# Optimization experiments

Measured on AMD Instinct MI355X. Metric: run time of the kernel, lower is better.

The kernel has to match this reference:

```python
import jax, jax.numpy as jnp
import numpy as np

B, N_MELS, T = 8, 96, 1024
FLUX = 1
N_DIMS = N_MELS * (1 + FLUX)          # 192
C = 32                                 # num_channels
D_MODEL = C * (N_DIMS // 4)            # 1536
N_LAYERS = 4
D_STATE = 16
D_CONV = 4
D_INNER = 2 * D_MODEL                  # 3072 (expand=2)
DT_RANK = -(-D_MODEL // 16)            # 96
N_CLASSES = 5


def setup_inputs() -> dict:
    key = jax.random.key(0)
    ks = iter(jax.random.split(key, 64))
    def rn(shape, scale=0.02):
        return jax.random.normal(next(ks), shape, dtype=jnp.float32) * scale
    p = {}
    p['x'] = jax.random.normal(next(ks), (B, N_MELS, T), dtype=jnp.float32)
    # ResidualBlock 1: conv3x3 -> act -> conv3x3, 1x1 shortcut (channel change 1->C)
    p['c1a_w'] = rn((C, 1, 3, 3)); p['c1a_b'] = jnp.zeros((C,), jnp.float32)
    p['c1b_w'] = rn((C, C, 3, 3)); p['c1b_b'] = jnp.zeros((C,), jnp.float32)
    p['c1s_w'] = rn((C, 1, 1, 1)); p['c1s_b'] = jnp.zeros((C,), jnp.float32)
    # ResidualBlock 2: identity shortcut (C->C)
    p['c2a_w'] = rn((C, C, 3, 3)); p['c2a_b'] = jnp.zeros((C,), jnp.float32)
    p['c2b_w'] = rn((C, C, 3, 3)); p['c2b_b'] = jnp.zeros((C,), jnp.float32)
    # Mamba layers (stacked over layer dim L)
    L = N_LAYERS
    p['norm_w'] = jnp.ones((L, D_MODEL), jnp.float32)
    p['in_w'] = rn((L, 2 * D_INNER, D_MODEL))
    p['conv_w'] = rn((L, D_INNER, D_CONV))
    p['conv_b'] = jnp.zeros((L, D_INNER), jnp.float32)
    p['xproj_w'] = rn((L, DT_RANK + 2 * D_STATE, D_INNER))
    p['dt_w'] = rn((L, D_INNER, DT_RANK))
    p['dt_b'] = rn((L, D_INNER), 0.01)
    A = jnp.tile(jnp.arange(1, D_STATE + 1, dtype=jnp.float32)[None], (D_INNER, 1))
    p['A_log'] = jnp.tile(jnp.log(A)[None], (L, 1, 1))
    p['Dp'] = jnp.ones((L, D_INNER), jnp.float32)
    p['out_w'] = rn((L, D_MODEL, D_INNER))
    p['fc_w'] = rn((N_CLASSES, D_MODEL)); p['fc_b'] = jnp.zeros((N_CLASSES,), jnp.float32)
    return p


def conv2d_same(x, w, b):
    y = jax.lax.conv_general_dilated(x, w, (1, 1), 'SAME',
                                     dimension_numbers=('NCHW', 'OIHW', 'NCHW'))
    return y + b[None, :, None, None]


def res_block(x, wa, ba, wb, bb, ws=None, bs=None):
    h = jax.nn.silu(conv2d_same(x, wa, ba))
    h = conv2d_same(h, wb, bb)
    sc = x if ws is None else conv2d_same(x, ws, bs)
    return jax.nn.silu(h + sc)


def maxpool_f2(x):
    # MaxPool2d(kernel=(2,1), stride=(2,1)) over (freq, time)
    return jax.lax.reduce_window(x, -jnp.inf, jax.lax.max,
                                 (1, 1, 2, 1), (1, 1, 2, 1), 'VALID')


def rmsnorm(x, w, eps=1e-5):
    return x * jax.lax.rsqrt(jnp.mean(x * x, -1, keepdims=True) + eps) * w


def mamba_layer(x, norm_w, in_w, conv_w, conv_b, xproj_w, dt_w, dt_b, A_log, Dp, out_w):
    # x: (B, T, D_MODEL)
    xn = rmsnorm(x, norm_w)
    xz = jnp.einsum('btd,ed->bte', xn, in_w)           # (B,T,2*d_inner)
    u, z = jnp.split(xz, 2, axis=-1)
    # depthwise causal conv over time
    u_t = jnp.transpose(u, (0, 2, 1))                   # (B, d_inner, T)
    u_t = jax.lax.conv_general_dilated(u_t, conv_w[:, None, :], (1,), [(D_CONV - 1, 0)],
                                       dimension_numbers=('NCH', 'OIH', 'NCH'),
                                       feature_group_count=D_INNER)
    u = jax.nn.silu(jnp.transpose(u_t, (0, 2, 1)) + conv_b)
    x_dbl = jnp.einsum('btd,ed->bte', u, xproj_w)
    dt, Bm, Cm = jnp.split(x_dbl, [DT_RANK, DT_RANK + D_STATE], axis=-1)
    delta = jax.nn.softplus(jnp.einsum('btr,dr->btd', dt, dt_w) + dt_b)  # (B,T,d_inner)
    A = -jnp.exp(A_log)                                 # (d_inner, d_state)

    def step(h, inp):
        d_t, u_tt, B_t, C_t = inp                        # (B,di),(B,di),(B,ds),(B,ds)
        dA = jnp.exp(d_t[..., None] * A)                 # (B, d_inner, d_state)
        h = dA * h + (d_t * u_tt)[..., None] * B_t[:, None, :]
        y = jnp.einsum('bds,bs->bd', h, C_t)
        return h, y

    h0 = jnp.zeros((x.shape[0], D_INNER, D_STATE), x.dtype)
    xs = (jnp.moveaxis(delta, 1, 0), jnp.moveaxis(u, 1, 0),
          jnp.moveaxis(Bm, 1, 0), jnp.moveaxis(Cm, 1, 0))
    _, ys = jax.lax.scan(step, h0, xs)
    y = jnp.moveaxis(ys, 0, 1) + u * Dp
    y = y * jax.nn.silu(z)
    return x + jnp.einsum('bte,de->btd', y, out_w)


def reference(x, c1a_w, c1a_b, c1b_w, c1b_b, c1s_w, c1s_b,
              c2a_w, c2a_b, c2b_w, c2b_b,
              norm_w, in_w, conv_w, conv_b, xproj_w, dt_w, dt_b, A_log, Dp, out_w,
              fc_w, fc_b):
    # flux: temporal diff, relu, left-pad on time, stack along freq
    diff = x[..., 1:] - x[..., :-1]
    diff = jax.nn.relu(jnp.pad(diff, ((0, 0), (0, 0), (1, 0))))
    h = jnp.concatenate([x, diff], axis=1)              # (B, n_dims, T)
    h = h[:, None]                                       # (B, 1, n_dims, T)
    h = maxpool_f2(res_block(h, c1a_w, c1a_b, c1b_w, c1b_b, c1s_w, c1s_b))
    h = maxpool_f2(res_block(h, c2a_w, c2a_b, c2b_w, c2b_b))
    h = h.reshape(h.shape[0], -1, h.shape[3])            # (B, C*(n_dims//4), T)
    h = jnp.transpose(h, (0, 2, 1))                      # (B, T, d_model)
    for l in range(N_LAYERS):
        h = mamba_layer(h, norm_w[l], in_w[l], conv_w[l], conv_b[l], xproj_w[l],
                        dt_w[l], dt_b[l], A_log[l], Dp[l], out_w[l])
    logits = jnp.einsum('btd,cd->btc', h, fc_w) + fc_b
    return jax.nn.silu(jnp.transpose(logits, (0, 2, 1)))  # (B, n_classes, T)
```

## Files before the change

kernel.cpp:

```cpp
#include <hip/hip_runtime.h>
#include <cstdint>
#include <cstddef>

#define DEV static __device__ __forceinline__

typedef unsigned short u16;
typedef unsigned int   u32;
typedef __bf16 bf16x8 __attribute__((ext_vector_type(8)));
typedef float  f32x4  __attribute__((ext_vector_type(4)));

namespace {
constexpr int NB     = 8;
constexpr int NT     = 1024;
constexpr int NMEL   = 96;
constexpr int NDIM   = 192;
constexpr int NCH    = 32;
constexpr int DMODEL = 1536;
constexpr int DINNER = 3072;
constexpr int DSTATE = 16;
constexpr int DTRANK = 96;
constexpr int NLAYER = 4;
constexpr int NCLASS = 5;
constexpr int MROWS  = NB * NT;
constexpr int NCHK   = 16;
constexpr int CHKT   = NT / NCHK;
}

DEV float siluf(float x)    { return x / (1.0f + __expf(-x)); }
DEV float softplusf(float x){ return fmaxf(x, 0.0f) + log1pf(__expf(-fabsf(x))); }

DEV u16 f2bf(float f) {
    u32 u = __float_as_uint(f);
    u32 r = u + 0x7FFFu + ((u >> 16) & 1u);
    return (u16)(r >> 16);
}
DEV float bf2f(u16 h) { return __uint_as_float(((u32)h) << 16); }

DEV f32x4 exp2v(f32x4 x) {
    f32x4 r;
    r[0] = exp2f(x[0]); r[1] = exp2f(x[1]);
    r[2] = exp2f(x[2]); r[3] = exp2f(x[3]);
    return r;
}

#define GLD(gp, lp) __builtin_amdgcn_global_load_lds( \
    (const __attribute__((address_space(1))) u32*)(const void*)(gp), \
    (__attribute__((address_space(3))) u32*)(void*)(lp), 16, 0, 0)

__global__ void k_zero(u16* p) { p[threadIdx.x] = 0; }

__global__ __launch_bounds__(256) void k_prep(const float* __restrict__ x,
                                              float* __restrict__ hcat)
{
    int idx = blockIdx.x * 256 + threadIdx.x;
    if (idx >= NB * NDIM * NT) return;
    int t = idx & (NT - 1);
    int m = (idx >> 10) % NDIM;
    int b = idx / (NDIM * NT);
    float v;
    if (m < NMEL) {
        v = x[((size_t)b * NMEL + m) * NT + t];
    } else {
        int mm = m - NMEL;
        v = 0.f;
        if (t > 0) {
            const float* p = x + ((size_t)b * NMEL + mm) * NT + t;
            v = fmaxf(p[0] - p[-1], 0.f);
        }
    }
    hcat[idx] = v;
}

__global__ __launch_bounds__(256) void k_wconv(const float* __restrict__ w,
    u16* __restrict__ dh, u16* __restrict__ dl)
{
    int idx = blockIdx.x * 256 + threadIdx.x;
    if (idx >= 9216) return;
    int ci = idx & 31, cout = (idx >> 5) & 31, tap = idx >> 10;
    float v = w[((size_t)cout * 32 + ci) * 9 + tap];
    u16 h = f2bf(v);
    dh[idx] = h;
    dl[idx] = f2bf(v - bf2f(h));
}

__global__ __launch_bounds__(256) void k_conv1a(const float* __restrict__ hcat,
    const float* __restrict__ w, const float* __restrict__ bias,
    u16* __restrict__ oh, u16* __restrict__ ol)
{
    int idx = blockIdx.x * 256 + threadIdx.x;
    if (idx >= NB * NDIM * NT) return;
    int t = idx & (NT - 1);
    int h = (idx >> 10) % NDIM;
    int b = idx / (NDIM * NT);
    float in[3][3];
    #pragma unroll
    for (int dh = 0; dh < 3; ++dh)
        #pragma unroll
        for (int dw = 0; dw < 3; ++dw) {
            int hh = h + dh - 1, tt = t + dw - 1;
            in[dh][dw] = (hh >= 0 && hh < NDIM && tt >= 0 && tt < NT)
                       ? hcat[((size_t)b * NDIM + hh) * NT + tt] : 0.f;
        }
    u16 hb[32], lb[32];
    #pragma unroll
    for (int c = 0; c < NCH; ++c) {
        float acc = bias[c];
        #pragma unroll
        for (int dh = 0; dh < 3; ++dh)
            #pragma unroll
            for (int dw = 0; dw < 3; ++dw)
                acc = fmaf(in[dh][dw], w[c * 9 + dh * 3 + dw], acc);
        float o = siluf(acc);
        u16 hh2 = f2bf(o);
        hb[c] = hh2;
        lb[c] = f2bf(o - bf2f(hh2));
    }
    size_t ob = (((size_t)b * NDIM + h) * NT + t) * 32;
    #pragma unroll
    for (int j = 0; j < 8; ++j) {
        ushort4 hv = { hb[j*4], hb[j*4+1], hb[j*4+2], hb[j*4+3] };
        ushort4 lv = { lb[j*4], lb[j*4+1], lb[j*4+2], lb[j*4+3] };
        *(ushort4*)(oh + ob + j * 4) = hv;
        *(ushort4*)(ol + ob + j * 4) = lv;
    }
}

template<int VAR>
__global__ __launch_bounds__(256) void k_convmfma(
    const u16* __restrict__ Xh, const u16* __restrict__ Xl,
    const u16* __restrict__ CWh, const u16* __restrict__ CWl,
    const float* __restrict__ hcat, const float* __restrict__ sw, const float* __restrict__ sb,
    const u16* __restrict__ Sh, const u16* __restrict__ Sl,
    const float* __restrict__ bias,
    u16* __restrict__ Oh, u16* __restrict__ Ol,
    float* __restrict__ RES,
    const u16* __restrict__ zeropad)
{
    constexpr int HIN = (VAR == 0) ? 192 : 96;
    __shared__ __align__(16) u16 lds[2][8448];
    const int t0 = blockIdx.x * 64;
    const int ho = blockIdx.y;
    const int b  = blockIdx.z;
    const int tid = threadIdx.x;
    const int wid = tid >> 6, lane = tid & 63;
    const int r0 = 2 * ho - 1;

    for (int cb = wid * 64; cb < 2112; cb += 256) {
        int c = cb + lane;
        int plane = (c >= 1056) ? 1 : 0;
        int cc = c - plane * 1056;
        int row = cc / 264;
        int rc  = cc - row * 264;
        int pos = rc >> 2;
        int slot = rc & 3;
        int cib = slot ^ ((pos >> 1) & 3);
        int h = r0 + row;
        int t = t0 - 1 + pos;
        const u16* bp = plane ? Xl : Xh;
        const u16* src = (h >= 0 && h < HIN && t >= 0 && t < NT)
            ? bp + (((size_t)(b * HIN + h)) * NT + t) * 32 + cib * 8
            : zeropad;
        u16* ldst = &lds[0][0] + (size_t)cb * 8;
        GLD(src, ldst);
    }
    __syncthreads();

    const int fr = lane & 15, fq = lane >> 4;
    f32x4 acc[2][2];
    #pragma unroll
    for (int pr = 0; pr < 2; ++pr)
        #pragma unroll
        for (int mt = 0; mt < 2; ++mt) acc[pr][mt] = (f32x4){0.f, 0.f, 0.f, 0.f};

    #pragma unroll
    for (int dh = 0; dh < 3; ++dh) {
        #pragma unroll
        for (int dt = 0; dt < 3; ++dt) {
            int tap = dh * 3 + dt;
            bf16x8 wh[2], wl[2];
            #pragma unroll
            for (int mt = 0; mt < 2; ++mt) {
                size_t wo = ((size_t)tap * 32 + mt * 16 + fr) * 32 + fq * 8;
                wh[mt] = *(const bf16x8*)(CWh + wo);
                wl[mt] = *(const bf16x8*)(CWl + wo);
            }
            int p = (wid << 4) + fr + dt;
            int sl = fq ^ ((p >> 1) & 3);
            #pragma unroll
            for (int pr = 0; pr < 2; ++pr) {
                int rr = pr + dh;
                const u16* lp = &lds[0][0] + ((rr * 66 + p) * 4 + sl) * 8;
                bf16x8 xh = *(const bf16x8*)lp;
                bf16x8 xl = *(const bf16x8*)(lp + 8448);
                #pragma unroll
                for (int mt = 0; mt < 2; ++mt) {
                    acc[pr][mt] = __builtin_amdgcn_mfma_f32_16x16x32_bf16(wh[mt], xh, acc[pr][mt], 0, 0, 0);
                    acc[pr][mt] = __builtin_amdgcn_mfma_f32_16x16x32_bf16(wh[mt], xl, acc[pr][mt], 0, 0, 0);
                    acc[pr][mt] = __builtin_amdgcn_mfma_f32_16x16x32_bf16(wl[mt], xh, acc[pr][mt], 0, 0, 0);
                }
            }
        }
    }

    const int t = t0 + (wid << 4) + fr;
    float hc0 = 0.f, hc1 = 0.f;
    if (VAR == 0) {
        hc0 = hcat[((size_t)(b * NDIM + 2 * ho    )) * NT + t];
        hc1 = hcat[((size_t)(b * NDIM + 2 * ho + 1)) * NT + t];
    }
    #pragma unroll
    for (int mt = 0; mt < 2; ++mt) {
        float v0[4], v1[4];
        if (VAR == 2) {
            ushort4 s0h = *(const ushort4*)(Sh + (((size_t)(b * 96 + 2 * ho    )) * NT + t) * 32 + mt * 16 + fq * 4);
            ushort4 s0l = *(const ushort4*)(Sl + (((size_t)(b * 96 + 2 * ho    )) * NT + t) * 32 + mt * 16 + fq * 4);
            ushort4 s1h = *(const ushort4*)(Sh + (((size_t)(b * 96 + 2 * ho + 1)) * NT + t) * 32 + mt * 16 + fq * 4);
            ushort4 s1l = *(const ushort4*)(Sl + (((size_t)(b * 96 + 2 * ho + 1)) * NT + t) * 32 + mt * 16 + fq * 4);
            v0[0] = bf2f(s0h.x) + bf2f(s0l.x); v0[1] = bf2f(s0h.y) + bf2f(s0l.y);
            v0[2] = bf2f(s0h.z) + bf2f(s0l.z); v0[3] = bf2f(s0h.w) + bf2f(s0l.w);
            v1[0] = bf2f(s1h.x) + bf2f(s1l.x); v1[1] = bf2f(s1h.y) + bf2f(s1l.y);
            v1[2] = bf2f(s1h.z) + bf2f(s1l.z); v1[3] = bf2f(s1h.w) + bf2f(s1l.w);
        }
        u16 hs[4], ls[4];
        float r0v[4], r1v[4];
        #pragma unroll
        for (int r = 0; r < 4; ++r) {
            int c = mt * 16 + fq * 4 + r;
            float a0 = acc[0][mt][r] + bias[c];
            float a1 = acc[1][mt][r] + bias[c];
            if (VAR == 0) {
                a0 += fmaf(hc0, sw[c], sb[c]);
                a1 += fmaf(hc1, sw[c], sb[c]);
            }
            if (VAR == 2) { a0 += v0[r]; a1 += v1[r]; }
            a0 = siluf(a0); a1 = siluf(a1);
            if (VAR == 1) { r0v[r] = a0; r1v[r] = a1; }
            else {
                float m = fmaxf(a0, a1);
                if (VAR == 2) r0v[r] = m;
                else { u16 hh = f2bf(m); hs[r] = hh; ls[r] = f2bf(m - bf2f(hh)); }
            }
        }
        if (VAR == 0) {
            size_t ob = (((size_t)(b * 96 + ho)) * NT + t) * 32 + mt * 16 + fq * 4;
            ushort4 hv = { hs[0], hs[1], hs[2], hs[3] };
            ushort4 lv = { ls[0], ls[1], ls[2], ls[3] };
            *(ushort4*)(Oh + ob) = hv;
            *(ushort4*)(Ol + ob) = lv;
        } else if (VAR == 1) {
            #pragma unroll
            for (int pr = 0; pr < 2; ++pr) {
                size_t ob = (((size_t)(b * 96 + 2 * ho + pr)) * NT + t) * 32 + mt * 16 + fq * 4;
                u16 hh[4], ll[4];
                #pragma unroll
                for (int r = 0; r < 4; ++r) {
                    float m = pr ? r1v[r] : r0v[r];
                    hh[r] = f2bf(m); ll[r] = f2bf(m - bf2f(hh[r]));
                }
                ushort4 hv = { hh[0], hh[1], hh[2], hh[3] };
                ushort4 lv = { ll[0], ll[1], ll[2], ll[3] };
                *(ushort4*)(Oh + ob) = hv;
                *(ushort4*)(Ol + ob) = lv;
            }
        } else {
            #pragma unroll
            for (int r = 0; r < 4; ++r) {
                int c = mt * 16 + fq * 4 + r;
                RES[((size_t)b * NT + t) * DMODEL + c * 48 + ho] = r0v[r];
            }
        }
    }
}

__global__ __launch_bounds__(256) void k_rmsnorm(const float* __restrict__ in,
    const float* __restrict__ w, u16* __restrict__ oh, u16* __restrict__ ol)
{
    int row = blockIdx.x;
    int tid = threadIdx.x;
    const float* p = in + (size_t)row * DMODEL;
    float v[6]; float ss = 0.f;
    #pragma unroll
    for (int j = 0; j < 6; ++j) { v[j] = p[tid + j * 256]; ss = fmaf(v[j], v[j], ss); }
    #pragma unroll
    for (int off = 1; off < 64; off <<= 1) ss += __shfl_xor(ss, off);
    __shared__ float red[4];
    int lane = tid & 63, wv = tid >> 6;
    if (lane == 0) red[wv] = ss;
    __syncthreads();
    float tot = red[0] + red[1] + red[2] + red[3];
    float sc = rsqrtf(tot * (1.0f / DMODEL) + 1e-5f);
    #pragma unroll
    for (int j = 0; j < 6; ++j) {
        int col = tid + j * 256;
        float xv = v[j] * sc * w[col];
        u16 h = f2bf(xv);
        oh[(size_t)row * DMODEL + col] = h;
        ol[(size_t)row * DMODEL + col] = f2bf(xv - bf2f(h));
    }
}

__global__ __launch_bounds__(256) void k_split(const float* __restrict__ src,
    u16* __restrict__ dh, u16* __restrict__ dl, int n4)
{
    int idx = blockIdx.x * 256 + threadIdx.x;
    if (idx >= n4) return;
    float4 v = ((const float4*)src)[idx];
    u16 h0 = f2bf(v.x), h1 = f2bf(v.y), h2 = f2bf(v.z), h3 = f2bf(v.w);
    u16 l0 = f2bf(v.x - bf2f(h0)), l1 = f2bf(v.y - bf2f(h1));
    u16 l2 = f2bf(v.z - bf2f(h2)), l3 = f2bf(v.w - bf2f(h3));
    uint2 hv = { (u32)h0 | ((u32)h1 << 16), (u32)h2 | ((u32)h3 << 16) };
    uint2 lv = { (u32)l0 | ((u32)l1 << 16), (u32)l2 | ((u32)l3 << 16) };
    ((uint2*)dh)[idx] = hv;
    ((uint2*)dl)[idx] = lv;
}

__global__ __launch_bounds__(256) void k_wsplit_pad(const float* __restrict__ src,
    u16* __restrict__ dh, u16* __restrict__ dl)
{
    int idx = blockIdx.x * 256 + threadIdx.x;
    if (idx >= DINNER * 128) return;
    int col = idx & 127, row = idx >> 7;
    float v = (col < DTRANK) ? src[(size_t)row * DTRANK + col] : 0.f;
    u16 h = f2bf(v);
    dh[idx] = h;
    dl[idx] = f2bf(v - bf2f(h));
}

template<int EPI>
__global__ __launch_bounds__(256) void k_gemm_mfma(
    const u16* __restrict__ Ahi, const u16* __restrict__ Alo, int lda,
    const u16* __restrict__ Bhi, const u16* __restrict__ Blo, int ldb,
    float* __restrict__ C, int ldc, int Ktot,
    const float* __restrict__ bias, size_t zStride)
{
    __shared__ __align__(16) u16 lds[4][8192];
    const int tid = threadIdx.x;
    const int m0 = blockIdx.y * 128, n0 = blockIdx.x * 128;
    const int kPer = Ktot / gridDim.z;
    const int kBase = blockIdx.z * kPer;
    const int wid = tid >> 6, lane = tid & 63;
    const int wr = wid >> 1, wc = wid & 1;
    const int fr = lane & 15, fq = lane >> 4;
    const int srow  = tid >> 3;
    const int sslot = (tid & 7) ^ ((tid >> 3) & 7);

    f32x4 acc[4][4];
    #pragma unroll
    for (int mi = 0; mi < 4; ++mi)
        #pragma unroll
        for (int ni = 0; ni < 4; ++ni) acc[mi][ni] = (f32x4){0.f, 0.f, 0.f, 0.f};

    for (int k0 = kBase; k0 < kBase + kPer; k0 += 64) {
        #pragma unroll
        for (int i = 0; i < 4; ++i) {
            int row = i * 32 + srow;
            size_t offA = (size_t)(m0 + row) * lda + k0 + sslot * 8;
            size_t offB = (size_t)(n0 + row) * ldb + k0 + sslot * 8;
            u16* lb = &lds[0][0] + i * 2048 + (wid << 9);
            GLD(Ahi + offA, lb);
            GLD(Alo + offA, lb + 8192);
            GLD(Bhi + offB, lb + 16384);
            GLD(Blo + offB, lb + 24576);
        }
        __syncthreads();
        #pragma unroll
        for (int h = 0; h < 2; ++h) {
            bf16x8 ah[4], al[4], bh[4], bl[4];
            #pragma unroll
            for (int mi = 0; mi < 4; ++mi) {
                int row = wr * 64 + mi * 16 + fr;
                int sl  = (h * 4 + fq) ^ (row & 7);
                const u16* p = &lds[0][row * 64 + sl * 8];
                ah[mi] = *(const bf16x8*)p;
                al[mi] = *(const bf16x8*)(p + 8192);
            }
            #pragma unroll
            for (int ni = 0; ni < 4; ++ni) {
                int row = wc * 64 + ni * 16 + fr;
                int sl  = (h * 4 + fq) ^ (row & 7);
                const u16* p = &lds[2][row * 64 + sl * 8];
                bh[ni] = *(const bf16x8*)p;
                bl[ni] = *(const bf16x8*)(p + 8192);
            }
            #pragma unroll
            for (int mi = 0; mi < 4; ++mi)
                #pragma unroll
                for (int ni = 0; ni < 4; ++ni) {
                    acc[mi][ni] = __builtin_amdgcn_mfma_f32_16x16x32_bf16(ah[mi], bh[ni], acc[mi][ni], 0, 0, 0);
                    acc[mi][ni] = __builtin_amdgcn_mfma_f32_16x16x32_bf16(ah[mi], bl[ni], acc[mi][ni], 0, 0, 0);
                    acc[mi][ni] = __builtin_amdgcn_mfma_f32_16x16x32_bf16(al[mi], bh[ni], acc[mi][ni], 0, 0, 0);
                }
        }
        __syncthreads();
    }

    float* Cz = C + (EPI == 0 ? (size_t)blockIdx.z * zStride : (size_t)0);
    #pragma unroll
    for (int mi = 0; mi < 4; ++mi)
        #pragma unroll
        for (int ni = 0; ni < 4; ++ni) {
            int gr = m0 + wr * 64 + mi * 16 + fq * 4;
            int gc = n0 + wc * 64 + ni * 16 + fr;
            float* cp = Cz + (size_t)gr * ldc + gc;
            #pragma unroll
            for (int r = 0; r < 4; ++r) {
                float v = acc[mi][ni][r];
                if (EPI == 1) v = softplusf(v + bias[gc]);
                if (EPI == 2) v += cp[(size_t)r * ldc];
                cp[(size_t)r * ldc] = v;
            }
        }
}

__global__ __launch_bounds__(256) void k_conv1d(
    const float* __restrict__ xz, const float* __restrict__ w,
    const float* __restrict__ bias, u16* __restrict__ uh, u16* __restrict__ ul)
{
    int idx = blockIdx.x * 256 + threadIdx.x;
    if (idx >= NB * NT * (DINNER / 4)) return;
    int dv = idx % (DINNER / 4);
    int t  = (idx / (DINNER / 4)) % NT;
    int b  = idx / ((DINNER / 4) * NT);
    int d  = dv * 4;
    const float* base = xz + ((size_t)b * NT + t) * (2 * DINNER) + d;
    float4 a[4];
    #pragma unroll
    for (int k = 0; k < 4; ++k) {
        int tm = t - 3 + k;
        if (tm >= 0) a[k] = *(const float4*)(base + (ptrdiff_t)(k - 3) * (2 * DINNER));
        else         a[k] = make_float4(0.f, 0.f, 0.f, 0.f);
    }
    float4 w0 = *(const float4*)(w + (size_t)(d + 0) * 4);
    float4 w1 = *(const float4*)(w + (size_t)(d + 1) * 4);
    float4 w2 = *(const float4*)(w + (size_t)(d + 2) * 4);
    float4 w3 = *(const float4*)(w + (size_t)(d + 3) * 4);
    float4 bb = *(const float4*)(bias + d);
    float o0 = siluf(bb.x + a[0].x * w0.x + a[1].x * w0.y + a[2].x * w0.z + a[3].x * w0.w);
    float o1 = siluf(bb.y + a[0].y * w1.x + a[1].y * w1.y + a[2].y * w1.z + a[3].y * w1.w);
    float o2 = siluf(bb.z + a[0].z * w2.x + a[1].z * w2.y + a[2].z * w2.z + a[3].z * w2.w);
    float o3 = siluf(bb.w + a[0].w * w3.x + a[1].w * w3.y + a[2].w * w3.z + a[3].w * w3.w);
    u16 h0 = f2bf(o0), h1 = f2bf(o1), h2 = f2bf(o2), h3 = f2bf(o3);
    u16 l0 = f2bf(o0 - bf2f(h0)), l1 = f2bf(o1 - bf2f(h1));
    u16 l2 = f2bf(o2 - bf2f(h2)), l3 = f2bf(o3 - bf2f(h3));
    size_t ob = ((size_t)b * NT + t) * DINNER + d;
    uint2 hv = { (u32)h0 | ((u32)h1 << 16), (u32)h2 | ((u32)h3 << 16) };
    uint2 lv = { (u32)l0 | ((u32)l1 << 16), (u32)l2 | ((u32)l3 << 16) };
    *(uint2*)(uh + ob) = hv;
    *(uint2*)(ul + ob) = lv;
}

__global__ __launch_bounds__(256) void k_reduce4(const float* __restrict__ part,
                                                 float* __restrict__ out)
{
    int idx = blockIdx.x * 256 + threadIdx.x;
    if (idx >= MROWS * 128) return;
    float s = part[idx] + part[(size_t)1 * MROWS * 128 + idx]
            + part[(size_t)2 * MROWS * 128 + idx] + part[(size_t)3 * MROWS * 128 + idx];
    out[idx] = s;
}

__global__ __launch_bounds__(256) void k_scan_p1(
    const float* __restrict__ xz, const u16* __restrict__ uh, const u16* __restrict__ ul,
    const float* __restrict__ xdbl, const float* __restrict__ A_log,
    float* __restrict__ HP, float* __restrict__ SS)
{
    const int d = blockIdx.x * 256 + threadIdx.x;
    const int c = blockIdx.y, b = blockIdx.z;
    const float L2E = 1.44269504088896340736f;
    f32x4 al0 = *(const f32x4*)(A_log + (size_t)d * DSTATE + 0);
    f32x4 al1 = *(const f32x4*)(A_log + (size_t)d * DSTATE + 4);
    f32x4 al2 = *(const f32x4*)(A_log + (size_t)d * DSTATE + 8);
    f32x4 al3 = *(const f32x4*)(A_log + (size_t)d * DSTATE + 12);
    f32x4 aa0, aa1, aa2, aa3;
    #pragma unroll
    for (int j = 0; j < 4; ++j) {
        aa0[j] = -__expf(al0[j]) * L2E;
        aa1[j] = -__expf(al1[j]) * L2E;
        aa2[j] = -__expf(al2[j]) * L2E;
        aa3[j] = -__expf(al3[j]) * L2E;
    }
    const int t0 = c * CHKT;
    const float* dP = xz + ((size_t)b * NT + t0) * (2 * DINNER) + d;
    const u16* uhP = uh + ((size_t)b * NT + t0) * DINNER + d;
    const u16* ulP = ul + ((size_t)b * NT + t0) * DINNER + d;
    const float* bP = xdbl + ((size_t)b * NT + t0) * 128 + DTRANK;
    f32x4 h0 = {0.f,0.f,0.f,0.f}, h1 = h0, h2 = h0, h3 = h0;
    float S = 0.f;
    float dlt = dP[0];
    float uu = bf2f(uhP[0]) + bf2f(ulP[0]);
    for (int t = 0; t < CHKT; ++t) {
        float dlt_n = 0.f, uu_n = 0.f;
        if (t + 1 < CHKT) {
            dlt_n = dP[2 * DINNER];
            uu_n = bf2f(uhP[DINNER]) + bf2f(ulP[DINNER]);
        }
        f32x4 B0 = *(const f32x4*)(bP + 0);
        f32x4 B1 = *(const f32x4*)(bP + 4);
        f32x4 B2 = *(const f32x4*)(bP + 8);
        f32x4 B3 = *(const f32x4*)(bP + 12);
        float du = dlt * uu;
        S += dlt;
        h0 = exp2v(dlt * aa0) * h0 + du * B0;
        h1 = exp2v(dlt * aa1) * h1 + du * B1;
        h2 = exp2v(dlt * aa2) * h2 + du * B2;
        h3 = exp2v(dlt * aa3) * h3 + du * B3;
        dP += 2 * DINNER; uhP += DINNER; ulP += DINNER; bP += 128;
        dlt = dlt_n; uu = uu_n;
    }
    size_t a = (((size_t)(b * NCHK + c) * DINNER) + d) * DSTATE;
    *(f32x4*)(HP + a + 0)  = h0;
    *(f32x4*)(HP + a + 4)  = h1;
    *(f32x4*)(HP + a + 8)  = h2;
    *(f32x4*)(HP + a + 12) = h3;
    SS[(size_t)(b * NCHK + c) * DINNER + d] = S;
}

__global__ __launch_bounds__(256) void k_scan_p2(float* __restrict__ HP,
    const float* __restrict__ SS, const float* __restrict__ A_log)
{
    int idx = blockIdx.x * 256 + threadIdx.x;
    if (idx >= NB * DINNER * DSTATE) return;
    int s = idx & (DSTATE - 1);
    int d = (idx >> 4) % DINNER;
    int b = idx / (DINNER * DSTATE);
    const float L2E = 1.44269504088896340736f;
    float aa = -__expf(A_log[d * DSTATE + s]) * L2E;
    float h = 0.f;
    #pragma unroll
    for (int c = 0; c < NCHK; ++c) {
        size_t a = (((size_t)(b * NCHK + c) * DINNER) + d) * DSTATE + s;
        float hc = HP[a];
        float P = exp2f(aa * SS[(size_t)(b * NCHK + c) * DINNER + d]);
        HP[a] = h;
        h = fmaf(P, h, hc);
    }
}

__global__ __launch_bounds__(256) void k_scan_p3(
    const float* __restrict__ xz,
    u16* uh, u16* ul,
    const float* __restrict__ xdbl,
    const float* __restrict__ A_log, const float* __restrict__ Dp,
    const float* __restrict__ HP)
{
    const int d = blockIdx.x * 256 + threadIdx.x;
    const int c = blockIdx.y, b = blockIdx.z;
    const float L2E = 1.44269504088896340736f;
    f32x4 al0 = *(const f32x4*)(A_log + (size_t)d * DSTATE + 0);
    f32x4 al1 = *(const f32x4*)(A_log + (size_t)d * DSTATE + 4);
    f32x4 al2 = *(const f32x4*)(A_log + (size_t)d * DSTATE + 8);
    f32x4 al3 = *(const f32x4*)(A_log + (size_t)d * DSTATE + 12);
    f32x4 aa0, aa1, aa2, aa3;
    #pragma unroll
    for (int j = 0; j < 4; ++j) {
        aa0[j] = -__expf(al0[j]) * L2E;
        aa1[j] = -__expf(al1[j]) * L2E;
        aa2[j] = -__expf(al2[j]) * L2E;
        aa3[j] = -__expf(al3[j]) * L2E;
    }
    const float dp = Dp[d];
    const int t0 = c * CHKT;
    const float* dP = xz + ((size_t)b * NT + t0) * (2 * DINNER) + d;
    const float* zP = dP + DINNER;
    const u16* uhP = uh + ((size_t)b * NT + t0) * DINNER + d;
    const u16* ulP = ul + ((size_t)b * NT + t0) * DINNER + d;
    u16* yhP = (u16*)uhP;
    u16* ylP = (u16*)ulP;
    const float* bP = xdbl + ((size_t)b * NT + t0) * 128 + DTRANK;
    size_t ha = (((size_t)(b * NCHK + c) * DINNER) + d) * DSTATE;
    f32x4 h0 = *(const f32x4*)(HP + ha + 0);
    f32x4 h1 = *(const f32x4*)(HP + ha + 4);
    f32x4 h2 = *(const f32x4*)(HP + ha + 8);
    f32x4 h3 = *(const f32x4*)(HP + ha + 12);
    float dlt = dP[0], zz = zP[0];
    float uu = bf2f(uhP[0]) + bf2f(ulP[0]);
    for (int t = 0; t < CHKT; ++t) {
        float dlt_n = 0.f, uu_n = 0.f, zz_n = 0.f;
        if (t + 1 < CHKT) {
            dlt_n = dP[2 * DINNER]; zz_n = zP[2 * DINNER];
            uu_n = bf2f(uhP[DINNER]) + bf2f(ulP[DINNER]);
        }
        f32x4 B0 = *(const f32x4*)(bP + 0);
        f32x4 B1 = *(const f32x4*)(bP + 4);
        f32x4 B2 = *(const f32x4*)(bP + 8);
        f32x4 B3 = *(const f32x4*)(bP + 12);
        f32x4 C0 = *(const f32x4*)(bP + DSTATE + 0);
        f32x4 C1 = *(const f32x4*)(bP + DSTATE + 4);
        f32x4 C2 = *(const f32x4*)(bP + DSTATE + 8);
        f32x4 C3 = *(const f32x4*)(bP + DSTATE + 12);
        float du = dlt * uu;
        h0 = exp2v(dlt * aa0) * h0 + du * B0;
        h1 = exp2v(dlt * aa1) * h1 + du * B1;
        h2 = exp2v(dlt * aa2) * h2 + du * B2;
        h3 = exp2v(dlt * aa3) * h3 + du * B3;
        f32x4 pv = h0 * C0 + h1 * C1 + h2 * C2 + h3 * C3;
        float p = (pv[0] + pv[1]) + (pv[2] + pv[3]);
        float yv = (p + uu * dp) * siluf(zz);
        u16 hh = f2bf(yv);
        yhP[0] = hh;
        ylP[0] = f2bf(yv - bf2f(hh));
        dP += 2 * DINNER; zP += 2 * DINNER;
        uhP += DINNER; ulP += DINNER; yhP += DINNER; ylP += DINNER;
        bP += 128;
        dlt = dlt_n; zz = zz_n; uu = uu_n;
    }
}

__global__ __launch_bounds__(256) void k_fc(const float* __restrict__ hR,
    const float* __restrict__ w, const float* __restrict__ bias,
    float* __restrict__ out)
{
    int row = blockIdx.x;
    int tid = threadIdx.x;
    const float* p = hR + (size_t)row * DMODEL;
    float acc[NCLASS] = {0.f, 0.f, 0.f, 0.f, 0.f};
    #pragma unroll
    for (int j = 0; j < 6; ++j) {
        int col = tid + j * 256;
        float v = p[col];
        #pragma unroll
        for (int c = 0; c < NCLASS; ++c)
            acc[c] = fmaf(v, w[c * DMODEL + col], acc[c]);
    }
    #pragma unroll
    for (int c = 0; c < NCLASS; ++c)
        #pragma unroll
        for (int off = 1; off < 64; off <<= 1)
            acc[c] += __shfl_xor(acc[c], off);
    __shared__ float red[4][NCLASS];
    int lane = tid & 63, wv = tid >> 6;
    if (lane == 0)
        for (int c = 0; c < NCLASS; ++c) red[wv][c] = acc[c];
    __syncthreads();
    if (tid < NCLASS) {
        float s = red[0][tid] + red[1][tid] + red[2][tid] + red[3][tid] + bias[tid];
        int b = row >> 10, t = row & (NT - 1);
        out[((size_t)b * NCLASS + tid) * NT + t] = siluf(s);
    }
}

extern "C" void kernel_launch(void* const* d_in, const int* in_sizes, int n_in,
                              void* d_out, int out_size, void* d_ws, size_t ws_size,
                              hipStream_t stream)
{
    const float* x      = (const float*)d_in[0];
    const float* c1a_w  = (const float*)d_in[1];
    const float* c1a_b  = (const float*)d_in[2];
    const float* c1b_w  = (const float*)d_in[3];
    const float* c1b_b  = (const float*)d_in[4];
    const float* c1s_w  = (const float*)d_in[5];
    const float* c1s_b  = (const float*)d_in[6];
    const float* c2a_w  = (const float*)d_in[7];
    const float* c2a_b  = (const float*)d_in[8];
    const float* c2b_w  = (const float*)d_in[9];
    const float* c2b_b  = (const float*)d_in[10];
    const float* norm_w = (const float*)d_in[11];
    const float* in_w   = (const float*)d_in[12];
    const float* conv_w = (const float*)d_in[13];
    const float* conv_b = (const float*)d_in[14];
    const float* xproj_w= (const float*)d_in[15];
    const float* dt_w   = (const float*)d_in[16];
    const float* dt_b   = (const float*)d_in[17];
    const float* A_log  = (const float*)d_in[18];
    const float* Dp     = (const float*)d_in[19];
    const float* out_w  = (const float*)d_in[20];
    const float* fc_w   = (const float*)d_in[21];
    const float* fc_b   = (const float*)d_in[22];
    float* outp = (float*)d_out;
    (void)in_sizes; (void)n_in; (void)out_size; (void)ws_size;

    char* base = (char*)d_ws;
    size_t off = 0;
    auto takeB = [&](size_t bytes) { void* p = base + off; off = (off + bytes + 255) & ~(size_t)255; return p; };
    float* HCAT = (float*)takeB((size_t)NB * NDIM * NT * 4);
    float* XZ   = (float*)takeB((size_t)MROWS * 2 * DINNER * 4);
    float* RES  = (float*)takeB((size_t)MROWS * DMODEL * 4);
    u16*   XNh  = (u16*)takeB((size_t)MROWS * DMODEL * 2);
    u16*   XNl  = (u16*)takeB((size_t)MROWS * DMODEL * 2);
    u16*   Uh   = (u16*)takeB((size_t)MROWS * DINNER * 2);
    u16*   Ul   = (u16*)takeB((size_t)MROWS * DINNER * 2);
    float* XDBL = (float*)takeB((size_t)MROWS * 128 * 4);
    float* XPART= (float*)takeB((size_t)4 * MROWS * 128 * 4);
    u16*   XDh  = (u16*)takeB((size_t)MROWS * 128 * 2);
    u16*   XDl  = (u16*)takeB((size_t)MROWS * 128 * 2);
    u16*   Wh   = (u16*)takeB((size_t)9437184 * 2);
    u16*   Wl   = (u16*)takeB((size_t)9437184 * 2);
    float* HP   = (float*)takeB((size_t)NB * NCHK * DINNER * DSTATE * 4);
    float* SS   = (float*)takeB((size_t)NB * NCHK * DINNER * 4);
    u16*   CW1h = (u16*)takeB(18432);
    u16*   CW1l = (u16*)takeB(18432);
    u16*   CW2h = (u16*)takeB(18432);
    u16*   CW2l = (u16*)takeB(18432);
    u16*   CW3h = (u16*)takeB(18432);
    u16*   CW3l = (u16*)takeB(18432);
    u16*   ZPAD = (u16*)takeB(256);

    u16* T1h = (u16*)XZ;
    u16* T1l = T1h + (size_t)NB * NDIM * NT * 32;
    u16* T3h = (u16*)XZ;
    u16* T3l = T3h + (size_t)NB * NDIM * NT * 32;
    u16* P1h = Uh;
    u16* P1l = Ul;

    const int n1 = NB * NDIM * NT;
    k_zero<<<1, 128, 0, stream>>>(ZPAD);
    k_prep  <<<(n1 + 255) / 256, 256, 0, stream>>>(x, HCAT);
    k_wconv<<<36, 256, 0, stream>>>(c1b_w, CW1h, CW1l);
    k_wconv<<<36, 256, 0, stream>>>(c2a_w, CW2h, CW2l);
    k_wconv<<<36, 256, 0, stream>>>(c2b_w, CW3h, CW3l);
    k_conv1a<<<(n1 + 255) / 256, 256, 0, stream>>>(HCAT, c1a_w, c1a_b, T1h, T1l);
    k_convmfma<0><<<dim3(16, 96, NB), 256, 0, stream>>>(
        T1h, T1l, CW1h, CW1l, HCAT, c1s_w, c1s_b, nullptr, nullptr,
        c1b_b, P1h, P1l, nullptr, ZPAD);
    k_convmfma<1><<<dim3(16, 48, NB), 256, 0, stream>>>(
        P1h, P1l, CW2h, CW2l, nullptr, nullptr, nullptr, nullptr, nullptr,
        c2a_b, T3h, T3l, nullptr, ZPAD);
    k_convmfma<2><<<dim3(16, 48, NB), 256, 0, stream>>>(
        T3h, T3l, CW3h, CW3l, nullptr, nullptr, nullptr, P1h, P1l,
        c2b_b, nullptr, nullptr, RES, ZPAD);

    for (int l = 0; l < NLAYER; ++l) {
        k_rmsnorm<<<MROWS, 256, 0, stream>>>(RES, norm_w + (size_t)l * DMODEL, XNh, XNl);
        k_split<<<(9437184 / 4 + 255) / 256, 256, 0, stream>>>(
            in_w + (size_t)l * 2 * DINNER * DMODEL, Wh, Wl, 9437184 / 4);
        k_gemm_mfma<0><<<dim3(2 * DINNER / 128, MROWS / 128, 1), 256, 0, stream>>>(
            XNh, XNl, DMODEL, Wh, Wl, DMODEL, XZ, 2 * DINNER, DMODEL, nullptr, 0);
        k_conv1d<<<(NB * NT * (DINNER / 4) + 255) / 256, 256, 0, stream>>>(
            XZ, conv_w + (size_t)l * DINNER * 4, conv_b + (size_t)l * DINNER, Uh, Ul);
        k_split<<<(393216 / 4 + 255) / 256, 256, 0, stream>>>(
            xproj_w + (size_t)l * 128 * DINNER, Wh, Wl, 393216 / 4);
        k_gemm_mfma<0><<<dim3(1, MROWS / 128, 4), 256, 0, stream>>>(
            Uh, Ul, DINNER, Wh, Wl, DINNER, XPART, 128, DINNER, nullptr, (size_t)MROWS * 128);
        k_reduce4<<<(MROWS * 128 + 255) / 256, 256, 0, stream>>>(XPART, XDBL);
        k_split<<<(MROWS * 128 / 4 + 255) / 256, 256, 0, stream>>>(XDBL, XDh, XDl, MROWS * 128 / 4);
        k_wsplit_pad<<<(DINNER * 128 + 255) / 256, 256, 0, stream>>>(
            dt_w + (size_t)l * DINNER * DTRANK, Wh, Wl);
        k_gemm_mfma<1><<<dim3(DINNER / 128, MROWS / 128, 1), 256, 0, stream>>>(
            XDh, XDl, 128, Wh, Wl, 128, XZ, 2 * DINNER, 128,
            dt_b + (size_t)l * DINNER, 0);
        k_scan_p1<<<dim3(DINNER / 256, NCHK, NB), 256, 0, stream>>>(
            XZ, Uh, Ul, XDBL, A_log + (size_t)l * DINNER * DSTATE, HP, SS);
        k_scan_p2<<<(NB * DINNER * DSTATE + 255) / 256, 256, 0, stream>>>(
            HP, SS, A_log + (size_t)l * DINNER * DSTATE);
        k_scan_p3<<<dim3(DINNER / 256, NCHK, NB), 256, 0, stream>>>(
            XZ, Uh, Ul, XDBL, A_log + (size_t)l * DINNER * DSTATE,
            Dp + (size_t)l * DINNER, HP);
        k_split<<<(4718592 / 4 + 255) / 256, 256, 0, stream>>>(
            out_w + (size_t)l * DMODEL * DINNER, Wh, Wl, 4718592 / 4);
        k_gemm_mfma<2><<<dim3(DMODEL / 128, MROWS / 128, 1), 256, 0, stream>>>(
            Uh, Ul, DINNER, Wh, Wl, DINNER, RES, DMODEL, DINNER, nullptr, 0);
    }
    k_fc<<<MROWS, 256, 0, stream>>>(RES, fc_w, fc_b, outp);
}
```

Before: 5.280 ms.

## Halve GEMM K-tile for occupancy, swizzle block order, retile depthwise conv1d over time

The split-bf16 MFMA GEMM now uses a 32-wide K step with half the LDS, an adjusted XOR swizzle and a launch-bounds hint of 4 blocks per CU, to allow more resident blocks. It also remaps block indices with a modulo-8 swizzle for better L2 locality. The depthwise conv1d now has each thread walk 16 consecutive timesteps for 2 channels, keeping a sliding window in registers instead of reloading 4 rows per output. The trade-off is twice as many barriers per K in the GEMM and possible register pressure under the new launch bound.

```diff
diff --git a/kernel.cpp b/kernel.cpp
--- a/kernel.cpp
+++ b/kernel.cpp
@@ -327,22 +327,27 @@
 }
 
 template<int EPI>
-__global__ __launch_bounds__(256) void k_gemm_mfma(
+__global__ __launch_bounds__(256, 4) void k_gemm_mfma(
     const u16* __restrict__ Ahi, const u16* __restrict__ Alo, int lda,
     const u16* __restrict__ Bhi, const u16* __restrict__ Blo, int ldb,
     float* __restrict__ C, int ldc, int Ktot,
     const float* __restrict__ bias, size_t zStride)
 {
-    __shared__ __align__(16) u16 lds[4][8192];
+    __shared__ __align__(16) u16 lds[4][4096];
     const int tid = threadIdx.x;
-    const int m0 = blockIdx.y * 128, n0 = blockIdx.x * 128;
+    const int nxy = gridDim.x * gridDim.y;
+    const int lin = blockIdx.y * gridDim.x + blockIdx.x;
+    const int swz = (lin & 7) * (nxy >> 3) + (lin >> 3);
+    const int bx = swz % gridDim.x;
+    const int by = swz / gridDim.x;
+    const int m0 = by * 128, n0 = bx * 128;
     const int kPer = Ktot / gridDim.z;
     const int kBase = blockIdx.z * kPer;
     const int wid = tid >> 6, lane = tid & 63;
     const int wr = wid >> 1, wc = wid & 1;
     const int fr = lane & 15, fq = lane >> 4;
-    const int srow  = tid >> 3;
-    const int sslot = (tid & 7) ^ ((tid >> 3) & 7);
+    const int srow  = tid >> 2;
+    const int sslot = (tid & 3) ^ ((srow >> 1) & 3);
 
     f32x4 acc[4][4];
     #pragma unroll
@@ -350,47 +355,44 @@
         #pragma unroll
         for (int ni = 0; ni < 4; ++ni) acc[mi][ni] = (f32x4){0.f, 0.f, 0.f, 0.f};
 
-    for (int k0 = kBase; k0 < kBase + kPer; k0 += 64) {
-        #pragma unroll
-        for (int i = 0; i < 4; ++i) {
-            int row = i * 32 + srow;
+    for (int k0 = kBase; k0 < kBase + kPer; k0 += 32) {
+        #pragma unroll
+        for (int i = 0; i < 2; ++i) {
+            int row = i * 64 + srow;
             size_t offA = (size_t)(m0 + row) * lda + k0 + sslot * 8;
             size_t offB = (size_t)(n0 + row) * ldb + k0 + sslot * 8;
             u16* lb = &lds[0][0] + i * 2048 + (wid << 9);
             GLD(Ahi + offA, lb);
-            GLD(Alo + offA, lb + 8192);
-            GLD(Bhi + offB, lb + 16384);
-            GLD(Blo + offB, lb + 24576);
+            GLD(Alo + offA, lb + 4096);
+            GLD(Bhi + offB, lb + 8192);
+            GLD(Blo + offB, lb + 12288);
         }
         __syncthreads();
-        #pragma unroll
-        for (int h = 0; h < 2; ++h) {
-            bf16x8 ah[4], al[4], bh[4], bl[4];
-            #pragma unroll
-            for (int mi = 0; mi < 4; ++mi) {
-                int row = wr * 64 + mi * 16 + fr;
-                int sl  = (h * 4 + fq) ^ (row & 7);
-                const u16* p = &lds[0][row * 64 + sl * 8];
-                ah[mi] = *(const bf16x8*)p;
-                al[mi] = *(const bf16x8*)(p + 8192);
-            }
+        bf16x8 ah[4], al[4], bh[4], bl[4];
+        #pragma unroll
+        for (int mi = 0; mi < 4; ++mi) {
+            int row = wr * 64 + mi * 16 + fr;
+            int sl  = fq ^ ((row >> 1) & 3);
+            const u16* p = &lds[0][row * 32 + sl * 8];
+            ah[mi] = *(const bf16x8*)p;
+            al[mi] = *(const bf16x8*)(p + 4096);
+        }
+        #pragma unroll
+        for (int ni = 0; ni < 4; ++ni) {
+            int row = wc * 64 + ni * 16 + fr;
+            int sl  = fq ^ ((row >> 1) & 3);
+            const u16* p = &lds[2][row * 32 + sl * 8];
+            bh[ni] = *(const bf16x8*)p;
+            bl[ni] = *(const bf16x8*)(p + 4096);
+        }
+        #pragma unroll
+        for (int mi = 0; mi < 4; ++mi)
             #pragma unroll
             for (int ni = 0; ni < 4; ++ni) {
-                int row = wc * 64 + ni * 16 + fr;
-                int sl  = (h * 4 + fq) ^ (row & 7);
-                const u16* p = &lds[2][row * 64 + sl * 8];
-                bh[ni] = *(const bf16x8*)p;
-                bl[ni] = *(const bf16x8*)(p + 8192);
+                acc[mi][ni] = __builtin_amdgcn_mfma_f32_16x16x32_bf16(ah[mi], bh[ni], acc[mi][ni], 0, 0, 0);
+                acc[mi][ni] = __builtin_amdgcn_mfma_f32_16x16x32_bf16(ah[mi], bl[ni], acc[mi][ni], 0, 0, 0);
+                acc[mi][ni] = __builtin_amdgcn_mfma_f32_16x16x32_bf16(al[mi], bh[ni], acc[mi][ni], 0, 0, 0);
             }
-            #pragma unroll
-            for (int mi = 0; mi < 4; ++mi)
-                #pragma unroll
-                for (int ni = 0; ni < 4; ++ni) {
-                    acc[mi][ni] = __builtin_amdgcn_mfma_f32_16x16x32_bf16(ah[mi], bh[ni], acc[mi][ni], 0, 0, 0);
-                    acc[mi][ni] = __builtin_amdgcn_mfma_f32_16x16x32_bf16(ah[mi], bl[ni], acc[mi][ni], 0, 0, 0);
-                    acc[mi][ni] = __builtin_amdgcn_mfma_f32_16x16x32_bf16(al[mi], bh[ni], acc[mi][ni], 0, 0, 0);
-                }
-        }
         __syncthreads();
     }
 
@@ -416,37 +418,33 @@
     const float* __restrict__ xz, const float* __restrict__ w,
     const float* __restrict__ bias, u16* __restrict__ uh, u16* __restrict__ ul)
 {
-    int idx = blockIdx.x * 256 + threadIdx.x;
-    if (idx >= NB * NT * (DINNER / 4)) return;
-    int dv = idx % (DINNER / 4);
-    int t  = (idx / (DINNER / 4)) % NT;
-    int b  = idx / ((DINNER / 4) * NT);
-    int d  = dv * 4;
-    const float* base = xz + ((size_t)b * NT + t) * (2 * DINNER) + d;
-    float4 a[4];
-    #pragma unroll
-    for (int k = 0; k < 4; ++k) {
-        int tm = t - 3 + k;
-        if (tm >= 0) a[k] = *(const float4*)(base + (ptrdiff_t)(k - 3) * (2 * DINNER));
-        else         a[k] = make_float4(0.f, 0.f, 0.f, 0.f);
-    }
-    float4 w0 = *(const float4*)(w + (size_t)(d + 0) * 4);
+    constexpr int CT = 16;
+    const int d  = (blockIdx.x * 256 + threadIdx.x) * 2;
+    const int t0 = blockIdx.y * CT;
+    const int b  = blockIdx.z;
+    float4 w0 = *(const float4*)(w + (size_t)d * 4);
     float4 w1 = *(const float4*)(w + (size_t)(d + 1) * 4);
-    float4 w2 = *(const float4*)(w + (size_t)(d + 2) * 4);
-    float4 w3 = *(const float4*)(w + (size_t)(d + 3) * 4);
-    float4 bb = *(const float4*)(bias + d);
-    float o0 = siluf(bb.x + a[0].x * w0.x + a[1].x * w0.y + a[2].x * w0.z + a[3].x * w0.w);
-    float o1 = siluf(bb.y + a[0].y * w1.x + a[1].y * w1.y + a[2].y * w1.z + a[3].y * w1.w);
-    float o2 = siluf(bb.z + a[0].z * w2.x + a[1].z * w2.y + a[2].z * w2.z + a[3].z * w2.w);
-    float o3 = siluf(bb.w + a[0].w * w3.x + a[1].w * w3.y + a[2].w * w3.z + a[3].w * w3.w);
-    u16 h0 = f2bf(o0), h1 = f2bf(o1), h2 = f2bf(o2), h3 = f2bf(o3);
-    u16 l0 = f2bf(o0 - bf2f(h0)), l1 = f2bf(o1 - bf2f(h1));
-    u16 l2 = f2bf(o2 - bf2f(h2)), l3 = f2bf(o3 - bf2f(h3));
-    size_t ob = ((size_t)b * NT + t) * DINNER + d;
-    uint2 hv = { (u32)h0 | ((u32)h1 << 16), (u32)h2 | ((u32)h3 << 16) };
-    uint2 lv = { (u32)l0 | ((u32)l1 << 16), (u32)l2 | ((u32)l3 << 16) };
-    *(uint2*)(uh + ob) = hv;
-    *(uint2*)(ul + ob) = lv;
+    float2 bb = *(const float2*)(bias + d);
+    const float* xp = xz + ((size_t)b * NT + t0) * (2 * DINNER) + d;
+    float2 a0 = {0.f, 0.f}, a1 = {0.f, 0.f}, a2 = {0.f, 0.f};
+    if (t0 > 0) {
+        a0 = *(const float2*)(xp - 3 * 2 * DINNER);
+        a1 = *(const float2*)(xp - 2 * 2 * DINNER);
+        a2 = *(const float2*)(xp - 1 * 2 * DINNER);
+    }
+    u32* uhp = (u32*)(uh + ((size_t)b * NT + t0) * DINNER + d);
+    u32* ulp = (u32*)(ul + ((size_t)b * NT + t0) * DINNER + d);
+    #pragma unroll
+    for (int t = 0; t < CT; ++t) {
+        float2 a3 = *(const float2*)(xp + (size_t)t * 2 * DINNER);
+        float o0 = siluf(bb.x + a0.x * w0.x + a1.x * w0.y + a2.x * w0.z + a3.x * w0.w);
+        float o1 = siluf(bb.y + a0.y * w1.x + a1.y * w1.y + a2.y * w1.z + a3.y * w1.w);
+        u16 h0 = f2bf(o0), h1 = f2bf(o1);
+        u16 l0 = f2bf(o0 - bf2f(h0)), l1 = f2bf(o1 - bf2f(h1));
+        uhp[(size_t)t * (DINNER / 2)] = (u32)h0 | ((u32)h1 << 16);
+        ulp[(size_t)t * (DINNER / 2)] = (u32)l0 | ((u32)l1 << 16);
+        a0 = a1; a1 = a2; a2 = a3;
+    }
 }
 
 __global__ __launch_bounds__(256) void k_reduce4(const float* __restrict__ part,
@@ -725,7 +723,7 @@
             in_w + (size_t)l * 2 * DINNER * DMODEL, Wh, Wl, 9437184 / 4);
         k_gemm_mfma<0><<<dim3(2 * DINNER / 128, MROWS / 128, 1), 256, 0, stream>>>(
             XNh, XNl, DMODEL, Wh, Wl, DMODEL, XZ, 2 * DINNER, DMODEL, nullptr, 0);
-        k_conv1d<<<(NB * NT * (DINNER / 4) + 255) / 256, 256, 0, stream>>>(
+        k_conv1d<<<dim3(DINNER / 512, NT / 16, NB), 256, 0, stream>>>(
             XZ, conv_w + (size_t)l * DINNER * 4, conv_b + (size_t)l * DINNER, Uh, Ul);
         k_split<<<(393216 / 4 + 255) / 256, 256, 0, stream>>>(
             xproj_w + (size_t)l * 128 * DINNER, Wh, Wl, 393216 / 4);
```

Result: slower. 5.424 ms (+2.7%).
